# Kernel optimization log

Measured on AMD Instinct MI355X. Metric: run time of the kernel, lower is better.

Reference implementation:

```python
import jax, jax.numpy as jnp
import numpy as np

B, S, D = 2, 2048, 1024
N, H = 16, 64  # n_heads, d_head
INIT_STD = 0.02
IGNORE = -100000.0


def setup_inputs() -> dict:
    key = jax.random.key(0)
    ks = jax.random.split(key, 6)
    return {
        "normalized_resid_pre": jax.random.normal(ks[0], (B, S, D), dtype=jnp.float32),
        "W_Q": jax.random.normal(ks[1], (N, D, H), dtype=jnp.float32) * INIT_STD,
        "W_K": jax.random.normal(ks[2], (N, D, H), dtype=jnp.float32) * INIT_STD,
        "W_V": jax.random.normal(ks[3], (N, D, H), dtype=jnp.float32) * INIT_STD,
        "W_O": jax.random.normal(ks[4], (N, H, D), dtype=jnp.float32) * INIT_STD,
        "b_Q": jnp.zeros((N, H), dtype=jnp.float32),
        "b_K": jnp.zeros((N, H), dtype=jnp.float32),
        "b_V": jnp.zeros((N, H), dtype=jnp.float32),
        "b_O": jnp.zeros((D,), dtype=jnp.float32),
    }


def reference(normalized_resid_pre, W_Q, W_K, W_V, W_O, b_Q, b_K, b_V, b_O):
    x = normalized_resid_pre
    q = jnp.einsum('ndh,bpd->bpnh', W_Q, x) + b_Q
    k = jnp.einsum('ndh,bpd->bpnh', W_K, x) + b_K
    v = jnp.einsum('ndh,bpd->bpnh', W_V, x) + b_V
    scores = jnp.einsum('bpnh,bsnh->bnps', q, k) / jnp.sqrt(jnp.float32(H))
    # causal mask: key_pos > query_pos -> IGNORE
    seq = scores.shape[-1]
    mask = jnp.triu(jnp.ones((seq, seq), dtype=bool), k=1)
    scores = jnp.where(mask, jnp.float32(IGNORE), scores)
    attn = jax.nn.softmax(scores, axis=-1)
    z = jnp.einsum('bnps,bsnh->bpnh', attn, v)
    # per-head out-proj then sum over heads
    out = jnp.einsum('bpnh,nhd->bpd', z, W_O) + b_O
    return out
```

## Files before the change

### kernel.cpp

```cpp
#include <hip/hip_runtime.h>
#include <math.h>

#define S_ 2048
#define D_ 1024
#define M_ 4096

typedef float f4 __attribute__((ext_vector_type(4)));
typedef float f16v __attribute__((ext_vector_type(16)));
typedef short s8v __attribute__((ext_vector_type(8)));
typedef unsigned short u16;

#define MFMA32(a,b,c) __builtin_amdgcn_mfma_f32_32x32x16_bf16((a),(b),(c),0,0,0)
#define QSCALE 0.1803368801111204f
#define NINF  -1e30f

__device__ __forceinline__ u16 f2bf(float x) {
    unsigned int u = __float_as_uint(x);
    u += 0x7fffu + ((u >> 16) & 1u);
    return (u16)(u >> 16);
}
__device__ __forceinline__ unsigned int cvtpk(float lo, float hi) {
    unsigned int r;
    asm("v_cvt_pk_bf16_f32 %0, %1, %2" : "=v"(r) : "v"(lo), "v"(hi));
    return r;
}
__device__ __forceinline__ void gload16(const void* g, void* l) {
    __builtin_amdgcn_global_load_lds(
        (const __attribute__((address_space(1))) unsigned int*)g,
        (__attribute__((address_space(3))) unsigned int*)l, 16, 0, 0);
}
union FragU { unsigned int u[4]; s8v v; };

__global__ __launch_bounds__(256) void prep_fused(
    const float* __restrict__ x,
    const float* __restrict__ Wq, const float* __restrict__ Wk, const float* __restrict__ Wv,
    const float* __restrict__ Wo,
    const float* __restrict__ bq, const float* __restrict__ bk, const float* __restrict__ bv,
    u16* __restrict__ xb, u16* __restrict__ Wc, u16* __restrict__ WoT,
    float* __restrict__ bc)
{
    __shared__ float t[64][65];
    const int bid = blockIdx.x;
    const int tid = threadIdx.x;

    if (bid < 2048) {
        int i = (bid * 256 + tid) * 8;
        f4 a = *(const f4*)(x + i);
        f4 b = *(const f4*)(x + i + 4);
        unsigned long long p0 =
            (unsigned long long)f2bf(a[0]) | ((unsigned long long)f2bf(a[1]) << 16) |
            ((unsigned long long)f2bf(a[2]) << 32) | ((unsigned long long)f2bf(a[3]) << 48);
        unsigned long long p1 =
            (unsigned long long)f2bf(b[0]) | ((unsigned long long)f2bf(b[1]) << 16) |
            ((unsigned long long)f2bf(b[2]) << 32) | ((unsigned long long)f2bf(b[3]) << 48);
        *(unsigned long long*)(xb + i)     = p0;
        *(unsigned long long*)(xb + i + 4) = p1;
    } else if (bid < 2816) {
        const int wb = bid - 2048;
        const int which = wb >> 8, n = (wb >> 4) & 15, dt = wb & 15;
        const float* W = which == 0 ? Wq : (which == 1 ? Wk : Wv);
        #pragma unroll
        for (int it = 0; it < 4; ++it) {
            int c = tid + it * 256;
            int d = c >> 4, h4 = c & 15;
            f4 v = *(const f4*)(W + ((size_t)n * 1024 + dt * 64 + d) * 64 + h4 * 4);
            #pragma unroll
            for (int j = 0; j < 4; ++j) t[h4 * 4 + j][d] = v[j];
        }
        __syncthreads();
        #pragma unroll
        for (int it = 0; it < 4; ++it) {
            int c = tid + it * 256;
            int h = c >> 4, d4 = c & 15;
            size_t o = (size_t)(which * 1024 + n * 64 + h) * 1024 + dt * 64 + d4 * 4;
            *(unsigned long long*)(Wc + o) =
                (unsigned long long)f2bf(t[h][d4 * 4 + 0]) |
                ((unsigned long long)f2bf(t[h][d4 * 4 + 1]) << 16) |
                ((unsigned long long)f2bf(t[h][d4 * 4 + 2]) << 32) |
                ((unsigned long long)f2bf(t[h][d4 * 4 + 3]) << 48);
        }
    } else if (bid < 3072) {
        const int ob = bid - 2816;
        const int rt = ob >> 4, ct = ob & 15;
        #pragma unroll
        for (int it = 0; it < 4; ++it) {
            int c = tid + it * 256;
            int r = c >> 4, c4 = c & 15;
            f4 v = *(const f4*)(Wo + (size_t)(rt * 64 + r) * 1024 + ct * 64 + c4 * 4);
            #pragma unroll
            for (int j = 0; j < 4; ++j) t[c4 * 4 + j][r] = v[j];
        }
        __syncthreads();
        #pragma unroll
        for (int it = 0; it < 4; ++it) {
            int c = tid + it * 256;
            int d = c >> 4, r4 = c & 15;
            size_t o = (size_t)(ct * 64 + d) * 1024 + rt * 64 + r4 * 4;
            *(unsigned long long*)(WoT + o) =
                (unsigned long long)f2bf(t[d][r4 * 4 + 0]) |
                ((unsigned long long)f2bf(t[d][r4 * 4 + 1]) << 16) |
                ((unsigned long long)f2bf(t[d][r4 * 4 + 2]) << 32) |
                ((unsigned long long)f2bf(t[d][r4 * 4 + 3]) << 48);
        }
    } else {
        int i = (bid - 3072) * 256 + tid;
        bc[i] = i < 1024 ? bq[i] : (i < 2048 ? bk[i - 1024] : bv[i - 2048]);
    }
}

template<int MODE>
__global__ __launch_bounds__(256) void gemm_bf16(
    const u16* __restrict__ A, const u16* __restrict__ B,
    const float* __restrict__ bias,
    u16* __restrict__ outq, u16* __restrict__ outk, u16* __restrict__ outvT,
    float* __restrict__ outf)
{
    __shared__ u16 sm[16384];
    u16* Ash = sm;
    u16* Bsh = sm + 8192;

    const int tid = threadIdx.x;
    const int lane = tid & 63, w = tid >> 6;
    const int wm = w & 1, wn = w >> 1;
    const int l31 = lane & 31, hi = lane >> 5;
    const int m0 = blockIdx.x * 128, n0 = blockIdx.y * 128;
    const int srow = lane >> 3;
    const int sc8 = (lane & 7) ^ srow;
    const int rx = l31 & 7;

    f16v acc[2][2];
    #pragma unroll
    for (int a = 0; a < 2; ++a)
        #pragma unroll
        for (int b = 0; b < 2; ++b)
            #pragma unroll
            for (int r = 0; r < 16; ++r) acc[a][b][r] = 0.f;

    for (int kt = 0; kt < 16; ++kt) {
        __syncthreads();
        #pragma unroll
        for (int i = 0; i < 4; ++i) {
            const int rb = (i * 4 + w) * 8;
            const int row = rb + srow;
            gload16(A + (size_t)(m0 + row) * 1024 + kt * 64 + sc8 * 8, Ash + rb * 64);
            gload16(B + (size_t)(n0 + row) * 1024 + kt * 64 + sc8 * 8, Bsh + rb * 64);
        }
        __syncthreads();
        #pragma unroll
        for (int ks = 0; ks < 4; ++ks) {
            s8v af[2], bf[2];
            #pragma unroll
            for (int mb = 0; mb < 2; ++mb)
                af[mb] = *(const s8v*)&Ash[(64 * wm + 32 * mb + l31) * 64 +
                                           ((2 * ks + hi) ^ rx) * 8];
            #pragma unroll
            for (int nb = 0; nb < 2; ++nb)
                bf[nb] = *(const s8v*)&Bsh[(64 * wn + 32 * nb + l31) * 64 +
                                           ((2 * ks + hi) ^ rx) * 8];
            #pragma unroll
            for (int mb = 0; mb < 2; ++mb)
                #pragma unroll
                for (int nb = 0; nb < 2; ++nb)
                    acc[mb][nb] = MFMA32(af[mb], bf[nb], acc[mb][nb]);
        }
    }

    __syncthreads();

    if constexpr (MODE == 0) {
        u16* Zw = sm + w * 4096;
        const int which = n0 >> 10;
        #pragma unroll
        for (int nb = 0; nb < 2; ++nb) {
            int nhl = 32 * nb + l31;
            float bv = bias[n0 + 64 * wn + nhl];
            #pragma unroll
            for (int mb = 0; mb < 2; ++mb)
                #pragma unroll
                for (int r = 0; r < 16; ++r) {
                    int ml = 32 * mb + (r & 3) + 8 * (r >> 2) + 4 * hi;
                    float vv = acc[mb][nb][r] + bv;
                    if (which == 0) vv *= QSCALE;
                    u16 hv = f2bf(vv);
                    int idx = (which == 2)
                        ? nhl * 64 + (ml ^ ((nhl & 7) << 3))
                        : ml * 64 + (nhl ^ ((ml & 7) << 3));
                    Zw[idx] = hv;
                }
        }
        __syncthreads();
        const int gmb = m0 + 64 * wm;
        const int gnb = n0 + 64 * wn;
        #pragma unroll
        for (int it = 0; it < 8; ++it) {
            int c = lane + it * 64;
            int row = c >> 3, c8 = c & 7;
            int idx = row * 64 + 8 * (c8 ^ (row & 7));
            s8v val = *(const s8v*)&Zw[idx];
            if (which == 0)
                *(s8v*)(outq + (size_t)(gmb + row) * 1024 + gnb + c8 * 8) = val;
            else if (which == 1)
                *(s8v*)(outk + (size_t)(gmb + row) * 1024 + (gnb - 1024) + c8 * 8) = val;
            else
                *(s8v*)(outvT + (size_t)(gnb - 2048 + row) * 4096 + gmb + c8 * 8) = val;
        }
    } else {
        #pragma unroll
        for (int nb = 0; nb < 2; ++nb) {
            int gcol = n0 + 64 * wn + 32 * nb + l31;
            float bv = bias[gcol];
            #pragma unroll
            for (int mb = 0; mb < 2; ++mb)
                #pragma unroll
                for (int r = 0; r < 16; ++r) {
                    int gm = m0 + 64 * wm + 32 * mb + (r & 3) + 8 * (r >> 2) + 4 * hi;
                    outf[(size_t)gm * 1024 + gcol] = acc[mb][nb][r] + bv;
                }
        }
    }
}

__global__ __launch_bounds__(128) void attn_mfma(
    const u16* __restrict__ qp, const u16* __restrict__ kp,
    const u16* __restrict__ vTp, u16* __restrict__ zp)
{
    __shared__ u16 sm[16384];
    const int tid = threadIdx.x;
    const int lane = tid & 63, w = tid >> 6;
    const int l31 = lane & 31, hi = lane >> 5;

    const int bid = blockIdx.x;
    const int lin = (bid & 7) * 128 + (bid >> 3);
    const int qt = 31 - (lin & 31);
    const int n = (lin >> 5) & 15, b = lin >> 9;

    const int q0 = qt * 64;
    const int qrow = q0 + 32 * w + l31;
    const int wqmin = q0 + 32 * w;
    const size_t mrow = (size_t)b * 2048 + qrow;
    const int srow = lane >> 3;
    const int sc8 = (lane & 7) ^ srow;
    const int rx = l31 & 7;

    s8v qf[4];
    #pragma unroll
    for (int c = 0; c < 4; ++c)
        qf[c] = *(const s8v*)(qp + mrow * 1024 + n * 64 + c * 16 + hi * 8);

    f16v acc[2];
    #pragma unroll
    for (int mb = 0; mb < 2; ++mb)
        #pragma unroll
        for (int r = 0; r < 16; ++r) acc[mb][r] = 0.f;
    float mrun = NINF, lrun = 0.f;
    const int nkt = qt + 1;

    auto STAGE = [&](int kt, int bufi) {
        u16* Kd = sm + bufi * 8192;
        u16* Vd = Kd + 4096;
        #pragma unroll
        for (int i = 0; i < 4; ++i) {
            const int rb = (i * 2 + w) * 8;
            const int row = rb + srow;
            gload16(kp + ((size_t)b * 2048 + kt * 64 + row) * 1024 + n * 64 + sc8 * 8,
                    Kd + rb * 64);
            gload16(vTp + ((size_t)n * 64 + row) * 4096 + b * 2048 + kt * 64 + sc8 * 8,
                    Vd + rb * 64);
        }
    };

    STAGE(0, 0);
    int cur = 0;
    for (int kt = 0; kt < nkt; ++kt) {
        __syncthreads();
        if (kt + 1 < nkt) STAGE(kt + 1, cur ^ 1);
        const u16* Kd = sm + cur * 8192;
        const u16* Vd = Kd + 4096;

        f16v sf[2];
        __builtin_amdgcn_s_setprio(1);
        #pragma unroll
        for (int t = 0; t < 2; ++t) {
            #pragma unroll
            for (int r = 0; r < 16; ++r) sf[t][r] = 0.f;
            const int row = 32 * t + l31;
            #pragma unroll
            for (int c = 0; c < 4; ++c) {
                s8v kf = *(const s8v*)&Kd[row * 64 + ((2 * c + hi) ^ rx) * 8];
                sf[t] = MFMA32(kf, qf[c], sf[t]);
            }
        }
        __builtin_amdgcn_s_setprio(0);

        if (64 * kt + 63 > wqmin) {
            #pragma unroll
            for (int t = 0; t < 2; ++t)
                #pragma unroll
                for (int r = 0; r < 16; ++r) {
                    const int sg = kt * 64 + 32 * t + (r & 3) + 8 * (r >> 2) + 4 * hi;
                    if (sg > qrow) sf[t][r] = NINF;
                }
        }

        float ma = NINF, mb2 = NINF, mc = NINF, md = NINF;
        #pragma unroll
        for (int t = 0; t < 2; ++t)
            #pragma unroll
            for (int r = 0; r < 16; r += 4) {
                ma  = fmaxf(ma,  sf[t][r]);
                mb2 = fmaxf(mb2, sf[t][r + 1]);
                mc  = fmaxf(mc,  sf[t][r + 2]);
                md  = fmaxf(md,  sf[t][r + 3]);
            }
        float mloc = fmaxf(fmaxf(ma, mb2), fmaxf(mc, md));
        mloc = fmaxf(mloc, __shfl_xor(mloc, 32, 64));

        float mbase;
        bool defer = (mloc - mrun <= 8.0f);
        if (__all(defer)) {
            mbase = mrun;
        } else {
            float mnew = fmaxf(mrun, mloc);
            float alpha = exp2f(mrun - mnew);
            lrun *= alpha;
            #pragma unroll
            for (int mb = 0; mb < 2; ++mb)
                #pragma unroll
                for (int r = 0; r < 16; ++r) acc[mb][r] *= alpha;
            mrun = mnew;
            mbase = mnew;
        }
        float sa = 0.f, sb = 0.f, sc2 = 0.f, sd = 0.f;
        #pragma unroll
        for (int t = 0; t < 2; ++t)
            #pragma unroll
            for (int r = 0; r < 16; r += 4) {
                float p0 = exp2f(sf[t][r]     - mbase);
                float p1 = exp2f(sf[t][r + 1] - mbase);
                float p2 = exp2f(sf[t][r + 2] - mbase);
                float p3 = exp2f(sf[t][r + 3] - mbase);
                sf[t][r] = p0; sf[t][r + 1] = p1;
                sf[t][r + 2] = p2; sf[t][r + 3] = p3;
                sa += p0; sb += p1; sc2 += p2; sd += p3;
            }
        float ls = (sa + sb) + (sc2 + sd);
        ls += __shfl_xor(ls, 32, 64);
        lrun += ls;

        s8v pf[4];
        #pragma unroll
        for (int c = 0; c < 4; ++c) {
            const int i0 = 2 * c, i1 = 2 * c + 1;
            const int t0 = i0 >> 2, u0 = i0 & 3;
            const int t1 = i1 >> 2, u1 = i1 & 3;
            unsigned int f00 = cvtpk(sf[t0][4 * u0 + 0], sf[t0][4 * u0 + 1]);
            unsigned int f01 = cvtpk(sf[t0][4 * u0 + 2], sf[t0][4 * u0 + 3]);
            unsigned int f10 = cvtpk(sf[t1][4 * u1 + 0], sf[t1][4 * u1 + 1]);
            unsigned int f11 = cvtpk(sf[t1][4 * u1 + 2], sf[t1][4 * u1 + 3]);
            unsigned int s0 = hi ? f00 : f10, s1 = hi ? f01 : f11;
            unsigned int r0 = __shfl_xor(s0, 32, 64);
            unsigned int r1 = __shfl_xor(s1, 32, 64);
            FragU f;
            f.u[0] = hi ? r0 : f00;  f.u[1] = hi ? r1 : f01;
            f.u[2] = hi ? f10 : r0;  f.u[3] = hi ? f11 : r1;
            pf[c] = f.v;
        }

        __builtin_amdgcn_s_setprio(1);
        #pragma unroll
        for (int mb = 0; mb < 2; ++mb) {
            const int row = 32 * mb + l31;
            #pragma unroll
            for (int c = 0; c < 4; ++c) {
                s8v vf = *(const s8v*)&Vd[row * 64 + ((2 * c + hi) ^ rx) * 8];
                acc[mb] = MFMA32(vf, pf[c], acc[mb]);
            }
        }
        __builtin_amdgcn_s_setprio(0);
        cur ^= 1;
    }

    __syncthreads();
    float linv = 1.0f / lrun;
    u16* Z = sm + w * 2048;
    #pragma unroll
    for (int mb = 0; mb < 2; ++mb)
        #pragma unroll
        for (int r = 0; r < 16; ++r) {
            int hcol = 32 * mb + (r & 3) + 8 * (r >> 2) + 4 * hi;
            int idx = l31 * 64 + (hcol ^ ((l31 & 7) << 3));
            Z[idx] = f2bf(acc[mb][r] * linv);
        }
    __syncthreads();
    #pragma unroll
    for (int it = 0; it < 4; ++it) {
        int c = lane + it * 64;
        int row = c >> 3, c8 = c & 7;
        int idx = row * 64 + 8 * (c8 ^ (row & 7));
        *(s8v*)(zp + ((size_t)b * 2048 + q0 + 32 * w + row) * 1024 + n * 64 + c8 * 8) =
            *(const s8v*)&Z[idx];
    }
}

extern "C" void kernel_launch(void* const* d_in, const int* in_sizes, int n_in,
                              void* d_out, int out_size, void* d_ws, size_t ws_size,
                              hipStream_t stream) {
    const float* x  = (const float*)d_in[0];
    const float* Wq = (const float*)d_in[1];
    const float* Wk = (const float*)d_in[2];
    const float* Wv = (const float*)d_in[3];
    const float* Wo = (const float*)d_in[4];
    const float* bq = (const float*)d_in[5];
    const float* bk = (const float*)d_in[6];
    const float* bv = (const float*)d_in[7];
    const float* bO = (const float*)d_in[8];
    float* out = (float*)d_out;

    char* p = (char*)d_ws;
    size_t o = 0;
    auto alloc = [&](size_t bytes) { char* r = p + o; o += bytes; return r; };
    const size_t MB8 = (size_t)M_ * D_ * 2;
    u16* xb   = (u16*)alloc(MB8);
    u16* Wc   = (u16*)alloc((size_t)3072 * 1024 * 2);
    u16* WoT  = (u16*)alloc((size_t)1024 * 1024 * 2);
    float* bc = (float*)alloc(65536);
    u16* qb   = (u16*)alloc(MB8);
    u16* kb   = (u16*)alloc(MB8);
    u16* vTb  = (u16*)alloc(MB8);
    if (ws_size < o) return;
    u16* zb = xb;

    prep_fused<<<3084, 256, 0, stream>>>(x, Wq, Wk, Wv, Wo, bq, bk, bv,
                                         xb, Wc, WoT, bc);
    gemm_bf16<0><<<dim3(32, 24), 256, 0, stream>>>(
        xb, Wc, bc, qb, kb, vTb, nullptr);
    attn_mfma<<<1024, 128, 0, stream>>>(qb, kb, vTb, zb);
    gemm_bf16<1><<<dim3(32, 8), 256, 0, stream>>>(
        zb, WoT, bO, nullptr, nullptr, nullptr, out);
}
```

Measured before the change: 248.4 us.

## Split causal attention into KV chunks with separate combine kernel

Replaces the per-64-query-tile attention kernel with a split-KV (flash-decoding style) scheme. Each block handles 128 queries with 4 waves over a chunk of up to 8 KV tiles, writing unnormalized partial outputs plus running max and sum, and a new combine kernel merges the chunks. The aim is to even out the load imbalance of causal attention and raise occupancy. It also remaps the QKV GEMM block index into an XCD-interleaved linear order. In exchange it adds a kernel launch, extra partial-output traffic, and stores partials rounded to bf16 before combining.

```diff
diff --git a/kernel.cpp b/kernel.cpp
--- a/kernel.cpp
+++ b/kernel.cpp
@@ -19,6 +19,9 @@
     u += 0x7fffu + ((u >> 16) & 1u);
     return (u16)(u >> 16);
 }
+__device__ __forceinline__ float bf2f(u16 h) {
+    return __uint_as_float(((unsigned int)h) << 16);
+}
 __device__ __forceinline__ unsigned int cvtpk(float lo, float hi) {
     unsigned int r;
     asm("v_cvt_pk_bf16_f32 %0, %1, %2" : "=v"(r) : "v"(lo), "v"(hi));
@@ -30,6 +33,16 @@
         (__attribute__((address_space(3))) unsigned int*)l, 16, 0, 0);
 }
 union FragU { unsigned int u[4]; s8v v; };
+union Pack8 { u16 h[8]; s8v v; };
+
+__device__ __constant__ unsigned char QT_OF[40] = {
+    0,1,2,3, 4,4, 5,5, 6,6, 7,7, 8,8,8, 9,9,9, 10,10,10, 11,11,11,
+    12,12,12,12, 13,13,13,13, 14,14,14,14, 15,15,15,15 };
+__device__ __constant__ unsigned char CK_OF[40] = {
+    0,0,0,0, 0,1, 0,1, 0,1, 0,1, 0,1,2, 0,1,2, 0,1,2, 0,1,2,
+    0,1,2,3, 0,1,2,3, 0,1,2,3, 0,1,2,3 };
+__device__ __constant__ unsigned char CUM[16] = {0,1,2,3,4,6,8,10,12,15,18,21,24,28,32,36};
+__device__ __constant__ unsigned char CC[16]  = {1,1,1,1,2,2,2,2,3,3,3,3,4,4,4,4};
 
 __global__ __launch_bounds__(256) void prep_fused(
     const float* __restrict__ x,
@@ -123,7 +136,15 @@
     const int lane = tid & 63, w = tid >> 6;
     const int wm = w & 1, wn = w >> 1;
     const int l31 = lane & 31, hi = lane >> 5;
-    const int m0 = blockIdx.x * 128, n0 = blockIdx.y * 128;
+    int m0, n0;
+    if constexpr (MODE == 0) {
+        const int lin = ((int)blockIdx.x & 7) * 96 + ((int)blockIdx.x >> 3);
+        m0 = (lin & 31) * 128;
+        n0 = (lin >> 5) * 128;
+    } else {
+        m0 = blockIdx.x * 128;
+        n0 = blockIdx.y * 128;
+    }
     const int srow = lane >> 3;
     const int sc8 = (lane & 7) ^ srow;
     const int rx = l31 & 7;
@@ -220,9 +241,10 @@
     }
 }
 
-__global__ __launch_bounds__(128) void attn_mfma(
+__global__ __launch_bounds__(256) void attn_chunk(
     const u16* __restrict__ qp, const u16* __restrict__ kp,
-    const u16* __restrict__ vTp, u16* __restrict__ zp)
+    const u16* __restrict__ vTp,
+    u16* __restrict__ pO, float* __restrict__ pm, float* __restrict__ pl)
 {
     __shared__ u16 sm[16384];
     const int tid = threadIdx.x;
@@ -230,13 +252,16 @@
     const int l31 = lane & 31, hi = lane >> 5;
 
     const int bid = blockIdx.x;
-    const int lin = (bid & 7) * 128 + (bid >> 3);
-    const int qt = 31 - (lin & 31);
-    const int n = (lin >> 5) & 15, b = lin >> 9;
-
-    const int q0 = qt * 64;
+    const int lin = (bid & 7) * 160 + (bid >> 3);
+    const int nb = lin / 40, cofs = lin % 40;
+    const int n = nb & 15, b = nb >> 4;
+    const int qt = QT_OF[cofs], ck = CK_OF[cofs];
+    const int kt0 = ck * 8;
+    const int kt1 = min(kt0 + 8, 2 * qt + 2);
+
+    const int q0 = qt * 128;
     const int qrow = q0 + 32 * w + l31;
-    const int wqmin = q0 + 32 * w;
+    const int wqmin = q0 + 32 * w, wqmax = wqmin + 31;
     const size_t mrow = (size_t)b * 2048 + qrow;
     const int srow = lane >> 3;
     const int sc8 = (lane & 7) ^ srow;
@@ -253,14 +278,13 @@
         #pragma unroll
         for (int r = 0; r < 16; ++r) acc[mb][r] = 0.f;
     float mrun = NINF, lrun = 0.f;
-    const int nkt = qt + 1;
 
     auto STAGE = [&](int kt, int bufi) {
         u16* Kd = sm + bufi * 8192;
         u16* Vd = Kd + 4096;
         #pragma unroll
-        for (int i = 0; i < 4; ++i) {
-            const int rb = (i * 2 + w) * 8;
+        for (int i = 0; i < 2; ++i) {
+            const int rb = (i * 4 + w) * 8;
             const int row = rb + srow;
             gload16(kp + ((size_t)b * 2048 + kt * 64 + row) * 1024 + n * 64 + sc8 * 8,
                     Kd + rb * 64);
@@ -269,119 +293,120 @@
         }
     };
 
-    STAGE(0, 0);
+    STAGE(kt0, 0);
     int cur = 0;
-    for (int kt = 0; kt < nkt; ++kt) {
+    for (int kt = kt0; kt < kt1; ++kt) {
         __syncthreads();
-        if (kt + 1 < nkt) STAGE(kt + 1, cur ^ 1);
-        const u16* Kd = sm + cur * 8192;
-        const u16* Vd = Kd + 4096;
-
-        f16v sf[2];
-        __builtin_amdgcn_s_setprio(1);
-        #pragma unroll
-        for (int t = 0; t < 2; ++t) {
-            #pragma unroll
-            for (int r = 0; r < 16; ++r) sf[t][r] = 0.f;
-            const int row = 32 * t + l31;
+        if (kt + 1 < kt1) STAGE(kt + 1, cur ^ 1);
+        if (64 * kt <= wqmax) {
+            const u16* Kd = sm + cur * 8192;
+            const u16* Vd = Kd + 4096;
+
+            f16v sf[2];
+            __builtin_amdgcn_s_setprio(1);
+            #pragma unroll
+            for (int t = 0; t < 2; ++t) {
+                #pragma unroll
+                for (int r = 0; r < 16; ++r) sf[t][r] = 0.f;
+                const int row = 32 * t + l31;
+                #pragma unroll
+                for (int c = 0; c < 4; ++c) {
+                    s8v kf = *(const s8v*)&Kd[row * 64 + ((2 * c + hi) ^ rx) * 8];
+                    sf[t] = MFMA32(kf, qf[c], sf[t]);
+                }
+            }
+            __builtin_amdgcn_s_setprio(0);
+
+            if (64 * kt + 63 > wqmin) {
+                #pragma unroll
+                for (int t = 0; t < 2; ++t)
+                    #pragma unroll
+                    for (int r = 0; r < 16; ++r) {
+                        const int sg = kt * 64 + 32 * t + (r & 3) + 8 * (r >> 2) + 4 * hi;
+                        if (sg > qrow) sf[t][r] = NINF;
+                    }
+            }
+
+            float ma = NINF, mb2 = NINF, mc = NINF, md = NINF;
+            #pragma unroll
+            for (int t = 0; t < 2; ++t)
+                #pragma unroll
+                for (int r = 0; r < 16; r += 4) {
+                    ma  = fmaxf(ma,  sf[t][r]);
+                    mb2 = fmaxf(mb2, sf[t][r + 1]);
+                    mc  = fmaxf(mc,  sf[t][r + 2]);
+                    md  = fmaxf(md,  sf[t][r + 3]);
+                }
+            float mloc = fmaxf(fmaxf(ma, mb2), fmaxf(mc, md));
+            mloc = fmaxf(mloc, __shfl_xor(mloc, 32, 64));
+
+            float mbase;
+            bool defer = (mloc - mrun <= 8.0f);
+            if (__all(defer)) {
+                mbase = mrun;
+            } else {
+                float mnew = fmaxf(mrun, mloc);
+                float alpha = exp2f(mrun - mnew);
+                lrun *= alpha;
+                #pragma unroll
+                for (int mb = 0; mb < 2; ++mb)
+                    #pragma unroll
+                    for (int r = 0; r < 16; ++r) acc[mb][r] *= alpha;
+                mrun = mnew;
+                mbase = mnew;
+            }
+            float sa = 0.f, sb = 0.f, sc2 = 0.f, sd = 0.f;
+            #pragma unroll
+            for (int t = 0; t < 2; ++t)
+                #pragma unroll
+                for (int r = 0; r < 16; r += 4) {
+                    float p0 = exp2f(sf[t][r]     - mbase);
+                    float p1 = exp2f(sf[t][r + 1] - mbase);
+                    float p2 = exp2f(sf[t][r + 2] - mbase);
+                    float p3 = exp2f(sf[t][r + 3] - mbase);
+                    sf[t][r] = p0; sf[t][r + 1] = p1;
+                    sf[t][r + 2] = p2; sf[t][r + 3] = p3;
+                    sa += p0; sb += p1; sc2 += p2; sd += p3;
+                }
+            float ls = (sa + sb) + (sc2 + sd);
+            ls += __shfl_xor(ls, 32, 64);
+            lrun += ls;
+
+            s8v pf[4];
             #pragma unroll
             for (int c = 0; c < 4; ++c) {
-                s8v kf = *(const s8v*)&Kd[row * 64 + ((2 * c + hi) ^ rx) * 8];
-                sf[t] = MFMA32(kf, qf[c], sf[t]);
+                const int i0 = 2 * c, i1 = 2 * c + 1;
+                const int t0 = i0 >> 2, u0 = i0 & 3;
+                const int t1 = i1 >> 2, u1 = i1 & 3;
+                unsigned int f00 = cvtpk(sf[t0][4 * u0 + 0], sf[t0][4 * u0 + 1]);
+                unsigned int f01 = cvtpk(sf[t0][4 * u0 + 2], sf[t0][4 * u0 + 3]);
+                unsigned int f10 = cvtpk(sf[t1][4 * u1 + 0], sf[t1][4 * u1 + 1]);
+                unsigned int f11 = cvtpk(sf[t1][4 * u1 + 2], sf[t1][4 * u1 + 3]);
+                unsigned int s0 = hi ? f00 : f10, s1 = hi ? f01 : f11;
+                unsigned int r0 = __shfl_xor(s0, 32, 64);
+                unsigned int r1 = __shfl_xor(s1, 32, 64);
+                FragU f;
+                f.u[0] = hi ? r0 : f00;  f.u[1] = hi ? r1 : f01;
+                f.u[2] = hi ? f10 : r0;  f.u[3] = hi ? f11 : r1;
+                pf[c] = f.v;
             }
-        }
-        __builtin_amdgcn_s_setprio(0);
-
-        if (64 * kt + 63 > wqmin) {
-            #pragma unroll
-            for (int t = 0; t < 2; ++t)
-                #pragma unroll
-                for (int r = 0; r < 16; ++r) {
-                    const int sg = kt * 64 + 32 * t + (r & 3) + 8 * (r >> 2) + 4 * hi;
-                    if (sg > qrow) sf[t][r] = NINF;
+
+            __builtin_amdgcn_s_setprio(1);
+            #pragma unroll
+            for (int mb = 0; mb < 2; ++mb) {
+                const int row = 32 * mb + l31;
+                #pragma unroll
+                for (int c = 0; c < 4; ++c) {
+                    s8v vf = *(const s8v*)&Vd[row * 64 + ((2 * c + hi) ^ rx) * 8];
+                    acc[mb] = MFMA32(vf, pf[c], acc[mb]);
                 }
-        }
-
-        float ma = NINF, mb2 = NINF, mc = NINF, md = NINF;
-        #pragma unroll
-        for (int t = 0; t < 2; ++t)
-            #pragma unroll
-            for (int r = 0; r < 16; r += 4) {
-                ma  = fmaxf(ma,  sf[t][r]);
-                mb2 = fmaxf(mb2, sf[t][r + 1]);
-                mc  = fmaxf(mc,  sf[t][r + 2]);
-                md  = fmaxf(md,  sf[t][r + 3]);
             }
-        float mloc = fmaxf(fmaxf(ma, mb2), fmaxf(mc, md));
-        mloc = fmaxf(mloc, __shfl_xor(mloc, 32, 64));
-
-        float mbase;
-        bool defer = (mloc - mrun <= 8.0f);
-        if (__all(defer)) {
-            mbase = mrun;
-        } else {
-            float mnew = fmaxf(mrun, mloc);
-            float alpha = exp2f(mrun - mnew);
-            lrun *= alpha;
-            #pragma unroll
-            for (int mb = 0; mb < 2; ++mb)
-                #pragma unroll
-                for (int r = 0; r < 16; ++r) acc[mb][r] *= alpha;
-            mrun = mnew;
-            mbase = mnew;
-        }
-        float sa = 0.f, sb = 0.f, sc2 = 0.f, sd = 0.f;
-        #pragma unroll
-        for (int t = 0; t < 2; ++t)
-            #pragma unroll
-            for (int r = 0; r < 16; r += 4) {
-                float p0 = exp2f(sf[t][r]     - mbase);
-                float p1 = exp2f(sf[t][r + 1] - mbase);
-                float p2 = exp2f(sf[t][r + 2] - mbase);
-                float p3 = exp2f(sf[t][r + 3] - mbase);
-                sf[t][r] = p0; sf[t][r + 1] = p1;
-                sf[t][r + 2] = p2; sf[t][r + 3] = p3;
-                sa += p0; sb += p1; sc2 += p2; sd += p3;
-            }
-        float ls = (sa + sb) + (sc2 + sd);
-        ls += __shfl_xor(ls, 32, 64);
-        lrun += ls;
-
-        s8v pf[4];
-        #pragma unroll
-        for (int c = 0; c < 4; ++c) {
-            const int i0 = 2 * c, i1 = 2 * c + 1;
-            const int t0 = i0 >> 2, u0 = i0 & 3;
-            const int t1 = i1 >> 2, u1 = i1 & 3;
-            unsigned int f00 = cvtpk(sf[t0][4 * u0 + 0], sf[t0][4 * u0 + 1]);
-            unsigned int f01 = cvtpk(sf[t0][4 * u0 + 2], sf[t0][4 * u0 + 3]);
-            unsigned int f10 = cvtpk(sf[t1][4 * u1 + 0], sf[t1][4 * u1 + 1]);
-            unsigned int f11 = cvtpk(sf[t1][4 * u1 + 2], sf[t1][4 * u1 + 3]);
-            unsigned int s0 = hi ? f00 : f10, s1 = hi ? f01 : f11;
-            unsigned int r0 = __shfl_xor(s0, 32, 64);
-            unsigned int r1 = __shfl_xor(s1, 32, 64);
-            FragU f;
-            f.u[0] = hi ? r0 : f00;  f.u[1] = hi ? r1 : f01;
-            f.u[2] = hi ? f10 : r0;  f.u[3] = hi ? f11 : r1;
-            pf[c] = f.v;
-        }
-
-        __builtin_amdgcn_s_setprio(1);
-        #pragma unroll
-        for (int mb = 0; mb < 2; ++mb) {
-            const int row = 32 * mb + l31;
-            #pragma unroll
-            for (int c = 0; c < 4; ++c) {
-                s8v vf = *(const s8v*)&Vd[row * 64 + ((2 * c + hi) ^ rx) * 8];
-                acc[mb] = MFMA32(vf, pf[c], acc[mb]);
-            }
-        }
-        __builtin_amdgcn_s_setprio(0);
+            __builtin_amdgcn_s_setprio(0);
+        }
         cur ^= 1;
     }
 
     __syncthreads();
-    float linv = 1.0f / lrun;
     u16* Z = sm + w * 2048;
     #pragma unroll
     for (int mb = 0; mb < 2; ++mb)
@@ -389,16 +414,68 @@
         for (int r = 0; r < 16; ++r) {
             int hcol = 32 * mb + (r & 3) + 8 * (r >> 2) + 4 * hi;
             int idx = l31 * 64 + (hcol ^ ((l31 & 7) << 3));
-            Z[idx] = f2bf(acc[mb][r] * linv);
-        }
+            Z[idx] = f2bf(acc[mb][r]);
+        }
+    if (hi == 0) {
+        pm[lin * 128 + 32 * w + l31] = mrun;
+        pl[lin * 128 + 32 * w + l31] = lrun;
+    }
     __syncthreads();
     #pragma unroll
     for (int it = 0; it < 4; ++it) {
         int c = lane + it * 64;
         int row = c >> 3, c8 = c & 7;
         int idx = row * 64 + 8 * (c8 ^ (row & 7));
-        *(s8v*)(zp + ((size_t)b * 2048 + q0 + 32 * w + row) * 1024 + n * 64 + c8 * 8) =
+        *(s8v*)(pO + (size_t)lin * 8192 + (32 * w + row) * 64 + c8 * 8) =
             *(const s8v*)&Z[idx];
+    }
+}
+
+__global__ __launch_bounds__(256) void attn_combine(
+    const u16* __restrict__ pO, const float* __restrict__ pm,
+    const float* __restrict__ pl, u16* __restrict__ zp)
+{
+    const int qtb = blockIdx.x;
+    const int qt = qtb & 15, nb = qtb >> 4;
+    const int n = nb & 15, b = nb >> 4;
+    const int cc = CC[qt];
+    const int base = nb * 40 + CUM[qt];
+    const int tid = threadIdx.x;
+    const int r = tid >> 1, hh = tid & 1;
+
+    float mi[4], wi[4];
+    float mg = NINF;
+    #pragma unroll
+    for (int i = 0; i < 4; ++i) {
+        mi[i] = (i < cc) ? pm[(base + i) * 128 + r] : NINF;
+        mg = fmaxf(mg, mi[i]);
+    }
+    float L = 0.f;
+    #pragma unroll
+    for (int i = 0; i < 4; ++i) {
+        wi[i] = exp2f(mi[i] - mg);
+        if (i < cc) L += pl[(base + i) * 128 + r] * wi[i];
+    }
+    const float inv = 1.0f / L;
+
+    #pragma unroll
+    for (int j = 0; j < 4; ++j) {
+        const int h0 = hh * 32 + j * 8;
+        float o[8] = {};
+        #pragma unroll
+        for (int i = 0; i < 4; ++i) {
+            if (i < cc) {
+                Pack8 v;
+                v.v = *(const s8v*)(pO + (size_t)(base + i) * 8192 + r * 64 + h0);
+                #pragma unroll
+                for (int k = 0; k < 8; ++k)
+                    o[k] += bf2f(v.h[k]) * wi[i];
+            }
+        }
+        Pack8 z;
+        #pragma unroll
+        for (int k = 0; k < 8; ++k) z.h[k] = f2bf(o[k] * inv);
+        *(s8v*)(zp + ((size_t)b * 2048 + qt * 128 + r) * 1024 + n * 64 + h0) = z.v;
     }
 }
 
@@ -427,14 +504,18 @@
     u16* qb   = (u16*)alloc(MB8);
     u16* kb   = (u16*)alloc(MB8);
     u16* vTb  = (u16*)alloc(MB8);
+    u16* pO   = (u16*)alloc((size_t)1280 * 8192 * 2);
+    float* pm = (float*)alloc((size_t)1280 * 128 * 4);
+    float* pl = (float*)alloc((size_t)1280 * 128 * 4);
     if (ws_size < o) return;
     u16* zb = xb;
 
     prep_fused<<<3084, 256, 0, stream>>>(x, Wq, Wk, Wv, Wo, bq, bk, bv,
                                          xb, Wc, WoT, bc);
-    gemm_bf16<0><<<dim3(32, 24), 256, 0, stream>>>(
+    gemm_bf16<0><<<768, 256, 0, stream>>>(
         xb, Wc, bc, qb, kb, vTb, nullptr);
-    attn_mfma<<<1024, 128, 0, stream>>>(qb, kb, vTb, zb);
+    attn_chunk<<<1280, 256, 0, stream>>>(qb, kb, vTb, pO, pm, pl);
+    attn_combine<<<512, 256, 0, stream>>>(pO, pm, pl, zb);
     gemm_bf16<1><<<dim3(32, 8), 256, 0, stream>>>(
         zb, WoT, bO, nullptr, nullptr, nullptr, out);
 }
```

Measured after the change: 217.4 us. 12.5% less time.
